# Kernel optimization log

Hardware: AMD Instinct MI355X
Metric: run time of the kernel (lower is better)

Reference implementation:

```python
import jax, jax.numpy as jnp
import numpy as np

N = 100000
E = 1600000
D_IN = 128
D_OUT = 64
NEG_SLOPE = 0.2
EPS = 1e-10


def setup_inputs() -> dict:
    key = jax.random.key(0)
    k1, k2, k3, k4, k5 = jax.random.split(key, 5)
    x = jax.random.normal(k1, (N, D_IN), dtype=jnp.float32)
    edge_index = jax.random.randint(k2, (2, E), 0, N, dtype=jnp.int64)
    edge_weight = jax.random.uniform(k3, (E,), dtype=jnp.float32)
    # Learned params: Linear weight (stored as [in, out] so Wh = x @ W) and attention vector a [2*out]
    W = jax.random.normal(k4, (D_IN, D_OUT), dtype=jnp.float32) / np.sqrt(D_IN)
    a = jax.random.normal(k5, (2 * D_OUT,), dtype=jnp.float32) * np.sqrt(2.0 / (2 * D_OUT))
    return {"x": x, "edge_index": edge_index, "edge_weight": edge_weight, "W": W, "a": a}


def reference(x, edge_index, edge_weight, W, a):
    n = x.shape[0]
    Wh = x @ W  # [N, D_OUT]
    src, tgt = edge_index[0], edge_index[1]
    # e_ij = LeakyReLU(a^T [Wh_i || Wh_j]) computed without materializing the concat:
    a_src, a_tgt = a[:D_OUT], a[D_OUT:]
    e = (Wh @ a_src)[src] + (Wh @ a_tgt)[tgt]  # [E]
    e = jnp.where(e > 0, e, NEG_SLOPE * e)
    e = e * edge_weight
    # segment softmax over incoming edges of each target node
    e_max = jax.ops.segment_max(e, tgt, num_segments=n)
    e_exp = jnp.exp(e - e_max[tgt])
    e_sum = jax.ops.segment_sum(e_exp, tgt, num_segments=n)
    alpha = e_exp / (e_sum[tgt] + EPS)
    # weighted scatter-add aggregation
    messages = alpha[:, None] * Wh[src]  # [E, D_OUT]
    out = jax.ops.segment_sum(messages, tgt, num_segments=n)
    return out
```

## Files before the change

kernel.cpp:

```cpp
#include <hip/hip_runtime.h>
#include <hip/hip_bf16.h>

#define DOUT 64
#define DIN 128
#define NEG_SLOPE 0.2f
#define EPSV 1e-10f
#define LDA 136
#define BKT_SHIFT 8
#define BKT_SIZE 256
#define NBMAX 512
#define PASSA_CHUNK 2048
#define CAP 12
#define CAP_B 5120

typedef __attribute__((ext_vector_type(8))) __bf16 bf16x8;
typedef __attribute__((ext_vector_type(8))) unsigned short ushortx8;
typedef __attribute__((ext_vector_type(4))) float floatx4;
typedef __attribute__((ext_vector_type(2))) float f32x2;

__device__ __forceinline__ float bf16_to_f32(unsigned short u) {
    return __uint_as_float(((unsigned int)u) << 16);
}
__device__ __forceinline__ f32x2 bf2_to_f32x2(unsigned int d) {
    f32x2 r;
    r.x = __uint_as_float(d << 16);
    r.y = __uint_as_float(d & 0xFFFF0000u);
    return r;
}
__device__ __forceinline__ unsigned short f32_to_bf16(float f) {
    __hip_bfloat16 h = __float2bfloat16(f);
    unsigned short u;
    __builtin_memcpy(&u, &h, 2);
    return u;
}
__device__ __forceinline__ unsigned int f32x2_to_bf16x2(float a, float b) {
    __hip_bfloat162 h = __float22bfloat162_rn(make_float2(a, b));
    unsigned int u;
    __builtin_memcpy(&u, &h, 4);
    return u;
}
__device__ __forceinline__ float leaky_exp(float vs, float vt, float w) {
    float v = vs + vt;
    v = (v > 0.f) ? v : NEG_SLOPE * v;
    return __expf(v * w);
}

__global__ __launch_bounds__(256) void gat_gemm_scores(
    const float* __restrict__ x, const float* __restrict__ W,
    const float* __restrict__ a, unsigned short* __restrict__ Wh,
    float* __restrict__ ssrc, float* __restrict__ stgt,
    int* __restrict__ cnt, int N)
{
    __shared__ unsigned short A_sh[64 * LDA];
    __shared__ unsigned short B_sh[64 * LDA];

    const int tid = threadIdx.x;
    const int rowbase = blockIdx.x * 64;

    if (blockIdx.x == 0) {
        cnt[tid] = 0;
        cnt[tid + 256] = 0;
    }

    for (int idx = tid; idx < DIN * DOUT; idx += 256) {
        int k = idx >> 6, n = idx & 63;
        B_sh[n * LDA + k] = f32_to_bf16(W[idx]);
    }
    for (int it = 0; it < 8; ++it) {
        int flat = it * 1024 + tid * 4;
        int row = flat >> 7, k = flat & 127;
        int grow = rowbase + row;
        float4 v = make_float4(0.f, 0.f, 0.f, 0.f);
        if (grow < N) v = *(const float4*)&x[(size_t)grow * DIN + k];
        uint2 packed = make_uint2(f32x2_to_bf16x2(v.x, v.y),
                                  f32x2_to_bf16x2(v.z, v.w));
        *(uint2*)&A_sh[row * LDA + k] = packed;
    }
    __syncthreads();

    const int lane = tid & 63;
    const int wv   = tid >> 6;
    const int c16  = lane & 15;
    const int quad = lane >> 4;

    floatx4 acc[4] = {floatx4{0,0,0,0}, floatx4{0,0,0,0},
                      floatx4{0,0,0,0}, floatx4{0,0,0,0}};

    const int arow = (wv * 16 + c16) * LDA;
    #pragma unroll
    for (int kk = 0; kk < 4; ++kk) {
        const int koff = kk * 32 + quad * 8;
        bf16x8 af = __builtin_bit_cast(bf16x8, *(const ushortx8*)&A_sh[arow + koff]);
        #pragma unroll
        for (int nt = 0; nt < 4; ++nt) {
            bf16x8 bf = __builtin_bit_cast(bf16x8,
                           *(const ushortx8*)&B_sh[(nt * 16 + c16) * LDA + koff]);
            acc[nt] = __builtin_amdgcn_mfma_f32_16x16x32_bf16(af, bf, acc[nt], 0, 0, 0);
        }
    }

    float asrc_v[4], atgt_v[4];
    #pragma unroll
    for (int nt = 0; nt < 4; ++nt) {
        asrc_v[nt] = a[nt * 16 + c16];
        atgt_v[nt] = a[64 + nt * 16 + c16];
    }
    const int rbase = rowbase + wv * 16 + quad * 4;
    #pragma unroll
    for (int r = 0; r < 4; ++r) {
        int row = rbase + r;
        if (row < N) {
            #pragma unroll
            for (int nt = 0; nt < 4; ++nt)
                Wh[(size_t)row * DOUT + nt * 16 + c16] = f32_to_bf16(acc[nt][r]);
        }
    }
    #pragma unroll
    for (int r = 0; r < 4; ++r) {
        float ps = 0.f, pt = 0.f;
        #pragma unroll
        for (int nt = 0; nt < 4; ++nt) {
            ps += acc[nt][r] * asrc_v[nt];
            pt += acc[nt][r] * atgt_v[nt];
        }
        #pragma unroll
        for (int m = 1; m < 16; m <<= 1) {
            ps += __shfl_xor(ps, m);
            pt += __shfl_xor(pt, m);
        }
        if (c16 == 0) {
            int row = rbase + r;
            if (row < N) { ssrc[row] = ps; stgt[row] = pt; }
        }
    }
}

__global__ __launch_bounds__(512) void gat_bin_scatter(
    const int* __restrict__ ei, const float* __restrict__ ew,
    int* __restrict__ cnt, int2* __restrict__ staged_g, int E)
{
    __shared__ int2 staged[NBMAX * CAP];
    __shared__ int fill[NBMAX];
    __shared__ int gpos[NBMAX];
    const int tid = threadIdx.x;
    if (tid < NBMAX) fill[tid] = 0;
    __syncthreads();

    const int base = blockIdx.x * PASSA_CHUNK;
    int e4 = base + tid * 4;
    if (e4 + 3 < E) {
        int4 ss = *(const int4*)&ei[e4];
        int4 tt = *(const int4*)&ei[E + e4];
        float4 ww = *(const float4*)&ew[e4];
        int sv[4] = {ss.x, ss.y, ss.z, ss.w};
        int tv[4] = {tt.x, tt.y, tt.z, tt.w};
        float wv4[4] = {ww.x, ww.y, ww.z, ww.w};
        #pragma unroll
        for (int u = 0; u < 4; ++u) {
            int b = tv[u] >> BKT_SHIFT;
            int2 rec = make_int2(sv[u] | ((tv[u] & (BKT_SIZE - 1)) << 17),
                                 __float_as_int(wv4[u]));
            int pos = atomicAdd(&fill[b], 1);
            if (pos < CAP) staged[b * CAP + pos] = rec;
            else {
                int gp = atomicAdd(&cnt[b], 1);
                if (gp < CAP_B) staged_g[(size_t)b * CAP_B + gp] = rec;
            }
        }
    } else {
        for (int e = e4; e < E && e < base + PASSA_CHUNK; ++e) {
            int s = ei[e], t = ei[E + e];
            int b = t >> BKT_SHIFT;
            int2 rec = make_int2(s | ((t & (BKT_SIZE - 1)) << 17),
                                 __float_as_int(ew[e]));
            int pos = atomicAdd(&fill[b], 1);
            if (pos < CAP) staged[b * CAP + pos] = rec;
            else {
                int gp = atomicAdd(&cnt[b], 1);
                if (gp < CAP_B) staged_g[(size_t)b * CAP_B + gp] = rec;
            }
        }
    }
    __syncthreads();

    if (tid < NBMAX) {
        int f = min(fill[tid], CAP);
        gpos[tid] = (f > 0) ? atomicAdd(&cnt[tid], f) : 0;
    }
    __syncthreads();

    for (int i = tid; i < NBMAX * CAP; i += 512) {
        int b = i / CAP;
        int r = i - b * CAP;
        if (r < min(fill[b], CAP)) {
            int gp = gpos[b] + r;
            if (gp < CAP_B) staged_g[(size_t)b * CAP_B + gp] = staged[i];
        }
    }
}

__global__ __launch_bounds__(512) void gat_binB_sort(
    const int2* __restrict__ staged_g, const int* __restrict__ cnt,
    const float* __restrict__ ssrc, const float* __restrict__ stgt,
    int* __restrict__ rbeg, int* __restrict__ rend,
    int2* __restrict__ sorted_sp, int N)
{
    __shared__ int2 rbuf[CAP_B];
    __shared__ int lcnt[512];
    __shared__ int lscan[512];
    __shared__ int lcur[BKT_SIZE];
    __shared__ float stgt_l[BKT_SIZE];

    const int b = blockIdx.x;
    const int tid = threadIdx.x;
    const int base = b * CAP_B;
    const int n = min(cnt[b], CAP_B);

    lcnt[tid] = 0;
    if (tid < BKT_SIZE) {
        int g = (b << BKT_SHIFT) + tid;
        stgt_l[tid] = (g < N) ? stgt[g] : 0.f;
    }
    __syncthreads();

    for (int i = tid; i < n; i += 512) {
        int2 r = staged_g[base + i];
        int s  = r.x & 0x1FFFF;
        int tl = (r.x >> 17) & (BKT_SIZE - 1);
        float p = leaky_exp(ssrc[s], stgt_l[tl], __int_as_float(r.y));
        rbuf[i] = make_int2(r.x, __float_as_int(p));
        atomicAdd(&lcnt[tl], 1);
    }
    __syncthreads();

    int c = lcnt[tid];
    lscan[tid] = c;
    __syncthreads();
    for (int off = 1; off < 256; off <<= 1) {
        int t = (tid >= off) ? lscan[tid - off] : 0;
        __syncthreads();
        lscan[tid] += t;
        __syncthreads();
    }
    if (tid < BKT_SIZE) {
        int excl = lscan[tid] - c;
        lcur[tid] = excl;
        int g = (b << BKT_SHIFT) + tid;
        if (g < N) { rbeg[g] = base + excl; rend[g] = base + excl + c; }
    }
    __syncthreads();

    for (int i = tid; i < n; i += 512) {
        int2 rec = rbuf[i];
        int tl = (rec.x >> 17) & (BKT_SIZE - 1);
        int pos = atomicAdd(&lcur[tl], 1);
        sorted_sp[base + pos] = make_int2(rec.x & 0x1FFFF, rec.y);
    }
}

__global__ __launch_bounds__(256) void gat_aggregate_csr(
    const int* __restrict__ rbeg, const int* __restrict__ rend,
    const int2* __restrict__ sorted_sp,
    const unsigned short* __restrict__ Wh, float* __restrict__ out, int N)
{
    int t = blockIdx.x * 4 + (threadIdx.x >> 6);
    if (t >= N) return;
    int lane = threadIdx.x & 63;
    int sub  = lane >> 3;
    int c8   = lane & 7;

    int beg = rbeg[t], end = rend[t];

    f32x2 acc2[4] = {f32x2{0.f,0.f}, f32x2{0.f,0.f},
                     f32x2{0.f,0.f}, f32x2{0.f,0.f}};
    float psum = 0.f;

    int i = beg + sub;
    for (; i + 8 < end; i += 16) {
        int2 spA = sorted_sp[i];
        int2 spB = sorted_sp[i + 8];
        float pA = __int_as_float(spA.y);
        float pB = __int_as_float(spB.y);
        uint4 wA = *(const uint4*)&Wh[(size_t)spA.x * DOUT + c8 * 8];
        uint4 wB = *(const uint4*)&Wh[(size_t)spB.x * DOUT + c8 * 8];
        f32x2 pA2 = {pA, pA}, pB2 = {pB, pB};
        acc2[0] += pA2 * bf2_to_f32x2(wA.x);
        acc2[1] += pA2 * bf2_to_f32x2(wA.y);
        acc2[2] += pA2 * bf2_to_f32x2(wA.z);
        acc2[3] += pA2 * bf2_to_f32x2(wA.w);
        psum += pA;
        acc2[0] += pB2 * bf2_to_f32x2(wB.x);
        acc2[1] += pB2 * bf2_to_f32x2(wB.y);
        acc2[2] += pB2 * bf2_to_f32x2(wB.z);
        acc2[3] += pB2 * bf2_to_f32x2(wB.w);
        psum += pB;
    }
    if (i < end) {
        int2 sp = sorted_sp[i];
        float p = __int_as_float(sp.y);
        uint4 w = *(const uint4*)&Wh[(size_t)sp.x * DOUT + c8 * 8];
        f32x2 p2 = {p, p};
        acc2[0] += p2 * bf2_to_f32x2(w.x);
        acc2[1] += p2 * bf2_to_f32x2(w.y);
        acc2[2] += p2 * bf2_to_f32x2(w.z);
        acc2[3] += p2 * bf2_to_f32x2(w.w);
        psum += p;
    }

    #pragma unroll
    for (int m = 8; m < 64; m <<= 1) {
        #pragma unroll
        for (int k = 0; k < 4; ++k) {
            acc2[k].x += __shfl_xor(acc2[k].x, m);
            acc2[k].y += __shfl_xor(acc2[k].y, m);
        }
        psum += __shfl_xor(psum, m);
    }

    if (sub == 0) {
        float inv = 1.0f / (psum + EPSV);
        float4 o0 = make_float4(acc2[0].x * inv, acc2[0].y * inv,
                                acc2[1].x * inv, acc2[1].y * inv);
        float4 o1 = make_float4(acc2[2].x * inv, acc2[2].y * inv,
                                acc2[3].x * inv, acc2[3].y * inv);
        *(float4*)&out[(size_t)t * DOUT + c8 * 8]     = o0;
        *(float4*)&out[(size_t)t * DOUT + c8 * 8 + 4] = o1;
    }
}

extern "C" void kernel_launch(void* const* d_in, const int* in_sizes, int n_in,
                              void* d_out, int out_size, void* d_ws, size_t ws_size,
                              hipStream_t stream) {
    const float* x  = (const float*)d_in[0];
    const int*   ei = (const int*)d_in[1];
    const float* ew = (const float*)d_in[2];
    const float* W  = (const float*)d_in[3];
    const float* a  = (const float*)d_in[4];
    const int N = in_sizes[0] / DIN;
    const int E = in_sizes[2];
    float* out = (float*)d_out;

    const int nbk = (N + BKT_SIZE - 1) >> BKT_SHIFT;

    char* wsb = (char*)d_ws;
    unsigned short* Wh = (unsigned short*)wsb;      wsb += (size_t)N * DOUT * 2;
    float* ssrc      = (float*)wsb;                 wsb += (size_t)N * 4;
    float* stgt      = (float*)wsb;                 wsb += (size_t)N * 4;
    int*   rbeg      = (int*)wsb;                   wsb += (size_t)N * 4;
    int*   rend      = (int*)wsb;                   wsb += (size_t)N * 4;
    int*   cnt       = (int*)wsb;                   wsb += NBMAX * 4;
    wsb = (char*)(((uintptr_t)wsb + 15) & ~(uintptr_t)15);
    int2*  staged_g  = (int2*)wsb;                  wsb += (size_t)nbk * CAP_B * 8;
    int2*  sorted_sp = (int2*)wsb;                  wsb += (size_t)nbk * CAP_B * 8;

    gat_gemm_scores<<<(N + 63) / 64, 256, 0, stream>>>(x, W, a, Wh, ssrc, stgt,
                                                       cnt, N);
    gat_bin_scatter<<<(E + PASSA_CHUNK - 1) / PASSA_CHUNK, 512, 0, stream>>>(
                  ei, ew, cnt, staged_g, E);
    gat_binB_sort<<<nbk, 512, 0, stream>>>(staged_g, cnt, ssrc, stgt,
                                           rbeg, rend, sorted_sp, N);
    gat_aggregate_csr<<<(N + 3) / 4, 256, 0, stream>>>(rbeg, rend, sorted_sp,
                                                       Wh, out, N);
}
```

Measured before the change: 198.8 us.

## Fuse GEMM-score and edge bin-scatter kernels into one role-split launch

Merges the dense x@W/score kernel and the edge bucket-scatter kernel into one 512-thread launch. Even blocks do the scatter, odd blocks do a 128-row GEMM tile, and the two roles share a union of their LDS layouts. This removes one kernel boundary and lets the memory-bound scatter overlap with the MFMA GEMM. Zeroing of the bucket counters moves to a hipMemsetAsync, which adds a small separate operation, and the larger LDS footprint per block may reduce occupancy.

```diff
diff --git a/kernel.cpp b/kernel.cpp
--- a/kernel.cpp
+++ b/kernel.cpp
@@ -45,156 +45,160 @@
     return __expf(v * w);
 }
 
-__global__ __launch_bounds__(256) void gat_gemm_scores(
+union FusedLDS {
+    struct {
+        unsigned short A_sh[128 * LDA];
+        unsigned short B_sh[64 * LDA];
+    } g;
+    struct {
+        int2 staged[NBMAX * CAP];
+        int  fill[NBMAX];
+        int  gpos[NBMAX];
+    } s;
+};
+
+__global__ __launch_bounds__(512) void gat_gemm_scatter(
     const float* __restrict__ x, const float* __restrict__ W,
     const float* __restrict__ a, unsigned short* __restrict__ Wh,
     float* __restrict__ ssrc, float* __restrict__ stgt,
-    int* __restrict__ cnt, int N)
+    const int* __restrict__ ei, const float* __restrict__ ew,
+    int* __restrict__ cnt, int2* __restrict__ staged_g, int N, int E)
 {
-    __shared__ unsigned short A_sh[64 * LDA];
-    __shared__ unsigned short B_sh[64 * LDA];
-
-    const int tid = threadIdx.x;
-    const int rowbase = blockIdx.x * 64;
-
-    if (blockIdx.x == 0) {
-        cnt[tid] = 0;
-        cnt[tid + 256] = 0;
-    }
-
-    for (int idx = tid; idx < DIN * DOUT; idx += 256) {
-        int k = idx >> 6, n = idx & 63;
-        B_sh[n * LDA + k] = f32_to_bf16(W[idx]);
-    }
-    for (int it = 0; it < 8; ++it) {
-        int flat = it * 1024 + tid * 4;
-        int row = flat >> 7, k = flat & 127;
-        int grow = rowbase + row;
-        float4 v = make_float4(0.f, 0.f, 0.f, 0.f);
-        if (grow < N) v = *(const float4*)&x[(size_t)grow * DIN + k];
-        uint2 packed = make_uint2(f32x2_to_bf16x2(v.x, v.y),
-                                  f32x2_to_bf16x2(v.z, v.w));
-        *(uint2*)&A_sh[row * LDA + k] = packed;
-    }
-    __syncthreads();
-
-    const int lane = tid & 63;
-    const int wv   = tid >> 6;
-    const int c16  = lane & 15;
-    const int quad = lane >> 4;
-
-    floatx4 acc[4] = {floatx4{0,0,0,0}, floatx4{0,0,0,0},
-                      floatx4{0,0,0,0}, floatx4{0,0,0,0}};
-
-    const int arow = (wv * 16 + c16) * LDA;
-    #pragma unroll
-    for (int kk = 0; kk < 4; ++kk) {
-        const int koff = kk * 32 + quad * 8;
-        bf16x8 af = __builtin_bit_cast(bf16x8, *(const ushortx8*)&A_sh[arow + koff]);
+    __shared__ FusedLDS u;
+    const int tid  = threadIdx.x;
+    const int role = blockIdx.x & 1;
+    const int id   = blockIdx.x >> 1;
+
+    if (role == 0) {
+        if (tid < NBMAX) u.s.fill[tid] = 0;
+        __syncthreads();
+
+        const int base = id * PASSA_CHUNK;
+        int e4 = base + tid * 4;
+        if (e4 + 3 < E) {
+            int4 ss = *(const int4*)&ei[e4];
+            int4 tt = *(const int4*)&ei[E + e4];
+            float4 ww = *(const float4*)&ew[e4];
+            int sv[4] = {ss.x, ss.y, ss.z, ss.w};
+            int tv[4] = {tt.x, tt.y, tt.z, tt.w};
+            float wv4[4] = {ww.x, ww.y, ww.z, ww.w};
+            #pragma unroll
+            for (int uu = 0; uu < 4; ++uu) {
+                int b = tv[uu] >> BKT_SHIFT;
+                int2 rec = make_int2(sv[uu] | ((tv[uu] & (BKT_SIZE - 1)) << 17),
+                                     __float_as_int(wv4[uu]));
+                int pos = atomicAdd(&u.s.fill[b], 1);
+                if (pos < CAP) u.s.staged[b * CAP + pos] = rec;
+                else {
+                    int gp = atomicAdd(&cnt[b], 1);
+                    if (gp < CAP_B) staged_g[(size_t)b * CAP_B + gp] = rec;
+                }
+            }
+        } else {
+            for (int e = e4; e < E && e < base + PASSA_CHUNK; ++e) {
+                int s = ei[e], t = ei[E + e];
+                int b = t >> BKT_SHIFT;
+                int2 rec = make_int2(s | ((t & (BKT_SIZE - 1)) << 17),
+                                     __float_as_int(ew[e]));
+                int pos = atomicAdd(&u.s.fill[b], 1);
+                if (pos < CAP) u.s.staged[b * CAP + pos] = rec;
+                else {
+                    int gp = atomicAdd(&cnt[b], 1);
+                    if (gp < CAP_B) staged_g[(size_t)b * CAP_B + gp] = rec;
+                }
+            }
+        }
+        __syncthreads();
+
+        if (tid < NBMAX) {
+            int f = min(u.s.fill[tid], CAP);
+            u.s.gpos[tid] = (f > 0) ? atomicAdd(&cnt[tid], f) : 0;
+        }
+        __syncthreads();
+
+        for (int i = tid; i < NBMAX * CAP; i += 512) {
+            int b = i / CAP;
+            int r = i - b * CAP;
+            if (r < min(u.s.fill[b], CAP)) {
+                int gp = u.s.gpos[b] + r;
+                if (gp < CAP_B) staged_g[(size_t)b * CAP_B + gp] = u.s.staged[i];
+            }
+        }
+    } else {
+        const int rowbase = id * 128;
+
+        for (int idx = tid; idx < DIN * DOUT; idx += 512) {
+            int k = idx >> 6, n = idx & 63;
+            u.g.B_sh[n * LDA + k] = f32_to_bf16(W[idx]);
+        }
+        #pragma unroll
+        for (int it = 0; it < 8; ++it) {
+            int flat = it * 2048 + tid * 4;
+            int row = flat >> 7, k = flat & 127;
+            int grow = rowbase + row;
+            float4 v = make_float4(0.f, 0.f, 0.f, 0.f);
+            if (grow < N) v = *(const float4*)&x[(size_t)grow * DIN + k];
+            uint2 packed = make_uint2(f32x2_to_bf16x2(v.x, v.y),
+                                      f32x2_to_bf16x2(v.z, v.w));
+            *(uint2*)&u.g.A_sh[row * LDA + k] = packed;
+        }
+        __syncthreads();
+
+        const int lane = tid & 63;
+        const int wv   = tid >> 6;
+        const int c16  = lane & 15;
+        const int quad = lane >> 4;
+
+        floatx4 acc[4] = {floatx4{0,0,0,0}, floatx4{0,0,0,0},
+                          floatx4{0,0,0,0}, floatx4{0,0,0,0}};
+
+        const int arow = (wv * 16 + c16) * LDA;
+        #pragma unroll
+        for (int kk = 0; kk < 4; ++kk) {
+            const int koff = kk * 32 + quad * 8;
+            bf16x8 af = __builtin_bit_cast(bf16x8,
+                           *(const ushortx8*)&u.g.A_sh[arow + koff]);
+            #pragma unroll
+            for (int nt = 0; nt < 4; ++nt) {
+                bf16x8 bf = __builtin_bit_cast(bf16x8,
+                               *(const ushortx8*)&u.g.B_sh[(nt * 16 + c16) * LDA + koff]);
+                acc[nt] = __builtin_amdgcn_mfma_f32_16x16x32_bf16(af, bf, acc[nt], 0, 0, 0);
+            }
+        }
+
+        float asrc_v[4], atgt_v[4];
         #pragma unroll
         for (int nt = 0; nt < 4; ++nt) {
-            bf16x8 bf = __builtin_bit_cast(bf16x8,
-                           *(const ushortx8*)&B_sh[(nt * 16 + c16) * LDA + koff]);
-            acc[nt] = __builtin_amdgcn_mfma_f32_16x16x32_bf16(af, bf, acc[nt], 0, 0, 0);
-        }
-    }
-
-    float asrc_v[4], atgt_v[4];
-    #pragma unroll
-    for (int nt = 0; nt < 4; ++nt) {
-        asrc_v[nt] = a[nt * 16 + c16];
-        atgt_v[nt] = a[64 + nt * 16 + c16];
-    }
-    const int rbase = rowbase + wv * 16 + quad * 4;
-    #pragma unroll
-    for (int r = 0; r < 4; ++r) {
-        int row = rbase + r;
-        if (row < N) {
+            asrc_v[nt] = a[nt * 16 + c16];
+            atgt_v[nt] = a[64 + nt * 16 + c16];
+        }
+        const int rbase = rowbase + wv * 16 + quad * 4;
+        #pragma unroll
+        for (int r = 0; r < 4; ++r) {
+            int row = rbase + r;
+            if (row < N) {
+                #pragma unroll
+                for (int nt = 0; nt < 4; ++nt)
+                    Wh[(size_t)row * DOUT + nt * 16 + c16] = f32_to_bf16(acc[nt][r]);
+            }
+        }
+        #pragma unroll
+        for (int r = 0; r < 4; ++r) {
+            float ps = 0.f, pt = 0.f;
             #pragma unroll
-            for (int nt = 0; nt < 4; ++nt)
-                Wh[(size_t)row * DOUT + nt * 16 + c16] = f32_to_bf16(acc[nt][r]);
-        }
-    }
-    #pragma unroll
-    for (int r = 0; r < 4; ++r) {
-        float ps = 0.f, pt = 0.f;
-        #pragma unroll
-        for (int nt = 0; nt < 4; ++nt) {
-            ps += acc[nt][r] * asrc_v[nt];
-            pt += acc[nt][r] * atgt_v[nt];
-        }
-        #pragma unroll
-        for (int m = 1; m < 16; m <<= 1) {
-            ps += __shfl_xor(ps, m);
-            pt += __shfl_xor(pt, m);
-        }
-        if (c16 == 0) {
-            int row = rbase + r;
-            if (row < N) { ssrc[row] = ps; stgt[row] = pt; }
-        }
-    }
-}
-
-__global__ __launch_bounds__(512) void gat_bin_scatter(
-    const int* __restrict__ ei, const float* __restrict__ ew,
-    int* __restrict__ cnt, int2* __restrict__ staged_g, int E)
-{
-    __shared__ int2 staged[NBMAX * CAP];
-    __shared__ int fill[NBMAX];
-    __shared__ int gpos[NBMAX];
-    const int tid = threadIdx.x;
-    if (tid < NBMAX) fill[tid] = 0;
-    __syncthreads();
-
-    const int base = blockIdx.x * PASSA_CHUNK;
-    int e4 = base + tid * 4;
-    if (e4 + 3 < E) {
-        int4 ss = *(const int4*)&ei[e4];
-        int4 tt = *(const int4*)&ei[E + e4];
-        float4 ww = *(const float4*)&ew[e4];
-        int sv[4] = {ss.x, ss.y, ss.z, ss.w};
-        int tv[4] = {tt.x, tt.y, tt.z, tt.w};
-        float wv4[4] = {ww.x, ww.y, ww.z, ww.w};
-        #pragma unroll
-        for (int u = 0; u < 4; ++u) {
-            int b = tv[u] >> BKT_SHIFT;
-            int2 rec = make_int2(sv[u] | ((tv[u] & (BKT_SIZE - 1)) << 17),
-                                 __float_as_int(wv4[u]));
-            int pos = atomicAdd(&fill[b], 1);
-            if (pos < CAP) staged[b * CAP + pos] = rec;
-            else {
-                int gp = atomicAdd(&cnt[b], 1);
-                if (gp < CAP_B) staged_g[(size_t)b * CAP_B + gp] = rec;
-            }
-        }
-    } else {
-        for (int e = e4; e < E && e < base + PASSA_CHUNK; ++e) {
-            int s = ei[e], t = ei[E + e];
-            int b = t >> BKT_SHIFT;
-            int2 rec = make_int2(s | ((t & (BKT_SIZE - 1)) << 17),
-                                 __float_as_int(ew[e]));
-            int pos = atomicAdd(&fill[b], 1);
-            if (pos < CAP) staged[b * CAP + pos] = rec;
-            else {
-                int gp = atomicAdd(&cnt[b], 1);
-                if (gp < CAP_B) staged_g[(size_t)b * CAP_B + gp] = rec;
-            }
-        }
-    }
-    __syncthreads();
-
-    if (tid < NBMAX) {
-        int f = min(fill[tid], CAP);
-        gpos[tid] = (f > 0) ? atomicAdd(&cnt[tid], f) : 0;
-    }
-    __syncthreads();
-
-    for (int i = tid; i < NBMAX * CAP; i += 512) {
-        int b = i / CAP;
-        int r = i - b * CAP;
-        if (r < min(fill[b], CAP)) {
-            int gp = gpos[b] + r;
-            if (gp < CAP_B) staged_g[(size_t)b * CAP_B + gp] = staged[i];
+            for (int nt = 0; nt < 4; ++nt) {
+                ps += acc[nt][r] * asrc_v[nt];
+                pt += acc[nt][r] * atgt_v[nt];
+            }
+            #pragma unroll
+            for (int m = 1; m < 16; m <<= 1) {
+                ps += __shfl_xor(ps, m);
+                pt += __shfl_xor(pt, m);
+            }
+            if (c16 == 0) {
+                int row = rbase + r;
+                if (row < N) { ssrc[row] = ps; stgt[row] = pt; }
+            }
         }
     }
 }
@@ -353,10 +357,14 @@
     int2*  staged_g  = (int2*)wsb;                  wsb += (size_t)nbk * CAP_B * 8;
     int2*  sorted_sp = (int2*)wsb;                  wsb += (size_t)nbk * CAP_B * 8;
 
-    gat_gemm_scores<<<(N + 63) / 64, 256, 0, stream>>>(x, W, a, Wh, ssrc, stgt,
-                                                       cnt, N);
-    gat_bin_scatter<<<(E + PASSA_CHUNK - 1) / PASSA_CHUNK, 512, 0, stream>>>(
-                  ei, ew, cnt, staged_g, E);
+    (void)hipMemsetAsync(cnt, 0, NBMAX * sizeof(int), stream);
+
+    const int g_scat = (E + PASSA_CHUNK - 1) / PASSA_CHUNK;
+    const int g_gemm = (N + 127) / 128;
+    const int g_tot = 2 * ((g_scat > g_gemm) ? g_scat : g_gemm);
+
+    gat_gemm_scatter<<<g_tot, 512, 0, stream>>>(x, W, a, Wh, ssrc, stgt,
+                                                ei, ew, cnt, staged_g, N, E);
     gat_binB_sort<<<nbk, 512, 0, stream>>>(staged_g, cnt, ssrc, stgt,
                                            rbeg, rend, sorted_sp, N);
     gat_aggregate_csr<<<(N + 3) / 4, 256, 0, stream>>>(rbeg, rend, sorted_sp,
```

New measurement: 188.4 us. -5.2%, faster.
